# Performance work log

Hardware: AMD Instinct MI355X
Metric: run time of the kernel (lower is better)

Reference implementation:

```python
import jax, jax.numpy as jnp
import numpy as np

S = 8192      # total packed tokens
H = 1152      # hidden size
NH = 16       # heads
HD = 72       # head dim
NSEG = 8      # number of packed (equal-length) sequences
L = S // NSEG # tokens per sequence
SCALE = HD ** -0.5


def setup_inputs() -> dict:
    key = jax.random.key(0)
    ks = jax.random.split(key, 4)
    hidden_states = jax.random.normal(ks[0], (1, S, H), jnp.float32)
    # Real rotary cos/sin per token position within each sequence.
    inv_freq = 1.0 / (10000.0 ** (np.arange(0, HD, 2, dtype=np.float64) / HD))
    freqs = np.outer(np.arange(L, dtype=np.float64), inv_freq)  # [L, HD/2]
    emb = np.concatenate([freqs, freqs], axis=-1)               # [L, HD]
    cos = jnp.asarray(np.tile(np.cos(emb), (NSEG, 1)), jnp.float32)  # [S, HD]
    sin = jnp.asarray(np.tile(np.sin(emb), (NSEG, 1)), jnp.float32)
    Wqkv = jax.random.normal(ks[1], (H, 3 * H), jnp.float32) * (H ** -0.5)
    bqkv = jnp.zeros((3 * H,), jnp.float32)
    Wout = jax.random.normal(ks[2], (H, H), jnp.float32) * (H ** -0.5)
    bout = jnp.zeros((H,), jnp.float32)
    cu_seqlens = jnp.arange(NSEG + 1, dtype=jnp.int32) * L
    return dict(hidden_states=hidden_states, cos=cos, sin=sin,
                Wqkv=Wqkv, bqkv=bqkv, Wout=Wout, bout=bout,
                cu_seqlens=cu_seqlens)


def _rotate_half(x):
    return jnp.concatenate([-x[..., HD // 2:], x[..., :HD // 2]], axis=-1)


def reference(hidden_states, cos, sin, Wqkv, bqkv, Wout, bout, cu_seqlens):
    # QKV projection (fused)
    qkv = hidden_states @ Wqkv + bqkv                 # [1, S, 3H]
    q, k, v = jnp.split(qkv, [H, 2 * H], axis=-1)
    q = q.reshape(1, S, NH, HD)
    k = k.reshape(1, S, NH, HD)
    v = v.reshape(1, S, NH, HD)
    # Inline RoPE on q/k (cos/sin broadcast over heads)
    c = cos[None, :, None, :]
    s = sin[None, :, None, :]
    q = q * c + _rotate_half(q) * s
    k = k * c + _rotate_half(k) * s
    # Varlen (block-diagonal) non-causal attention: equal-length segments
    q = q.reshape(NSEG, L, NH, HD)
    k = k.reshape(NSEG, L, NH, HD)
    v = v.reshape(NSEG, L, NH, HD)
    scores = jnp.einsum('nqhd,nkhd->nhqk', q, k) * SCALE  # [NSEG, NH, L, L]
    probs = jax.nn.softmax(scores, axis=-1)
    ctx = jnp.einsum('nhqk,nkhd->nqhd', probs, v)         # [NSEG, L, NH, HD]
    ctx = ctx.reshape(1, S, H)
    # Output projection
    return ctx @ Wout + bout
```

## Files before the change

### kernel.cpp

```cpp
#include <hip/hip_runtime.h>
#include <hip/hip_fp16.h>
#include <cstdint>

typedef _Float16 half8 __attribute__((ext_vector_type(8)));
typedef _Float16 half4 __attribute__((ext_vector_type(4)));
typedef float floatx4 __attribute__((ext_vector_type(4)));

#define S_TOT 8192
#define H_DIM 1152
#define NHEAD 16
#define HD 72
#define QSTR 96
#define KSTR 104
#define PSTR 76
#define VSTR 76
#define VT_TILE 6080
#define NSEG 8
#define SEGL 1024
#define QSCALE 0.17002324631230988f

__device__ __forceinline__ void gld_lds16(const void* g, void* l) {
  __builtin_amdgcn_global_load_lds((const __attribute__((address_space(1))) void*)g,
                                   (__attribute__((address_space(3))) void*)l, 16, 0, 0);
}

__global__ void cast_f32_f16(const float* __restrict__ in, _Float16* __restrict__ out, int n) {
  int i = (blockIdx.x * 256 + threadIdx.x) * 4;
  if (i < n) {
    float4 v = *(const float4*)(in + i);
    half4 o = { (_Float16)v.x, (_Float16)v.y, (_Float16)v.z, (_Float16)v.w };
    *(half4*)(out + i) = o;
  }
}

__global__ void transpose_cast(const float* __restrict__ W, _Float16* __restrict__ Wt,
                               int R, int C) {
  __shared__ float tile[32][33];
  int tx = threadIdx.x, ty = threadIdx.y;
  int bx = blockIdx.x, by = blockIdx.y;
#pragma unroll
  for (int i = 0; i < 4; ++i)
    tile[ty + i * 8][tx] = W[(size_t)(by * 32 + ty + i * 8) * C + bx * 32 + tx];
  __syncthreads();
#pragma unroll
  for (int i = 0; i < 4; ++i)
    Wt[(size_t)(bx * 32 + ty + i * 8) * R + by * 32 + tx] = (_Float16)tile[tx][ty + i * 8];
}

template <bool OUT_HALF>
__global__ __launch_bounds__(512, 2) void gemm256(
    const _Float16* __restrict__ A, const _Float16* __restrict__ Bt,
    const float* __restrict__ bias, float* __restrict__ Cf, _Float16* __restrict__ Ch,
    int M, int N, int K, int NT) {
  extern __shared__ half8 smem8[];
  char* smem = (char*)smem8;
  const int tid = threadIdx.x;
  const int lane = tid & 63;
  const int w = tid >> 6;
  const int quad = lane >> 4, l16 = lane & 15;
  const int wm = w >> 2, wn = w & 3;

  const int orig = blockIdx.x;
  const int xcd = orig & 7, widx = orig >> 3;
  const int mt = xcd * 4 + (widx & 3), nt = widx >> 2;
  const int m0 = mt * 256, n0 = nt * 256;

  const _Float16* pA[2];
  const _Float16* pB[2];
#pragma unroll
  for (int i = 0; i < 2; ++i) {
    int c = i * 512 + tid;
    int r = c >> 2, cs = c & 3;
    int col = ((cs ^ ((r >> 1) & 3)) << 3);
    pA[i] = A + (size_t)(m0 + r) * K + col;
    int br = n0 + r; if (br >= N) br = N - 1;
    pB[i] = Bt + (size_t)br * K + col;
  }
  const int st0 = tid * 16, st1 = tid * 16 + 8192;
  const int rsl = ((quad ^ ((l16 >> 1) & 3)) << 4);
  const int aoff = (wm * 128 + l16) * 64 + rsl;
  const int boff = 16384 + (wn * 64 + l16) * 64 + rsl;

  half8 afA[8], bfA[4], afB[8], bfB[4];
  floatx4 acc[8][4] = {};

#define STG_A(ds, kcol) { \
  gld_lds16(pA[0] + (kcol), smem + (ds) * 32768 + st0); \
  gld_lds16(pA[1] + (kcol), smem + (ds) * 32768 + st1); }
#define STG_B(ds, kcol) { \
  gld_lds16(pB[0] + (kcol), smem + (ds) * 32768 + 16384 + st0); \
  gld_lds16(pB[1] + (kcol), smem + (ds) * 32768 + 16384 + st1); }
#define LDB4(s, bfx) { \
  _Pragma("unroll") for (int in = 0; in < 4; ++in) \
    bfx[in] = *(const half8*)(smem + (s) * 32768 + boff + in * 1024); }
#define LDA8(s, afx) { \
  _Pragma("unroll") for (int j = 0; j < 8; ++j) \
    afx[j] = *(const half8*)(smem + (s) * 32768 + aoff + j * 1024); }
#define MFMA32(afx, bfx) { \
  __builtin_amdgcn_s_setprio(1); \
  _Pragma("unroll") for (int j = 0; j < 8; ++j) \
  _Pragma("unroll") for (int in = 0; in < 4; ++in) \
    acc[j][in] = \
      __builtin_amdgcn_mfma_f32_16x16x32_f16(afx[j], bfx[in], acc[j][in], 0, 0, 0); \
  __builtin_amdgcn_s_setprio(0); }
#define BAR() __builtin_amdgcn_s_barrier()
#define SBAR() __builtin_amdgcn_sched_barrier(0)
#define LGKM0() { asm volatile("s_waitcnt lgkmcnt(0)" ::: "memory"); SBAR(); }
#define VMWAIT(t) { \
  if ((t) + 3 < KT)        { asm volatile("s_waitcnt vmcnt(4)" ::: "memory"); } \
  else if ((t) + 3 == KT)  { asm volatile("s_waitcnt vmcnt(0)" ::: "memory"); } }

  STG_A(0, 0);  STG_B(0, 0);
  STG_A(1, 32); STG_B(1, 32);
  STG_A(2, 64); STG_B(2, 64);
  asm volatile("s_waitcnt vmcnt(4)" ::: "memory");
  BAR();
  LDB4(0, bfA); LDA8(0, afA);
  LGKM0();

  const int KT = K >> 5;
#pragma unroll 1
  for (int u = 0; u < KT; u += 2) {
    {
      const int rs = (u + 1) & 3, ws = (u + 3) & 3;
      LDB4(rs, bfB); LDA8(rs, afB);
      if (u + 3 < KT) { STG_A(ws, (u + 3) * 32); STG_B(ws, (u + 3) * 32); }
      SBAR();
      MFMA32(afA, bfA);
      SBAR();
      LGKM0();
      VMWAIT(u);
      BAR();
    }
    {
      const int rs = (u + 2) & 3, ws = (u + 4) & 3;
      if (u + 2 < KT) { LDB4(rs, bfA); LDA8(rs, afA); }
      if (u + 4 < KT) { STG_A(ws, (u + 4) * 32); STG_B(ws, (u + 4) * 32); }
      SBAR();
      MFMA32(afB, bfB);
      SBAR();
      LGKM0();
      VMWAIT(u + 1);
      if (u + 2 < KT) BAR();
    }
  }
#undef STG_A
#undef STG_B
#undef LDB4
#undef LDA8
#undef MFMA32
#undef BAR
#undef SBAR
#undef LGKM0
#undef VMWAIT

#pragma unroll
  for (int im = 0; im < 8; ++im) {
    int m = m0 + wm * 128 + im * 16 + quad * 4;
#pragma unroll
    for (int in = 0; in < 4; ++in) {
      int n = n0 + wn * 64 + in * 16 + l16;
      if (n < N) {
        float b = bias[n];
#pragma unroll
        for (int r = 0; r < 4; ++r) {
          float v = acc[im][in][r] + b;
          if (OUT_HALF) Ch[(size_t)(m + r) * N + n] = (_Float16)v;
          else          Cf[(size_t)(m + r) * N + n] = v;
        }
      }
    }
  }
}

__global__ void rope_scatter(const _Float16* __restrict__ QKV,
                             const float* __restrict__ cosb,
                             const float* __restrict__ sinb,
                             _Float16* __restrict__ Qo, _Float16* __restrict__ Ko) {
  int t = blockIdx.x * 256 + threadIdx.x;
  int l = t & 1023, h = (t >> 10) & 15, n = t >> 14;
  int s = n * SEGL + l;
  const _Float16* q = QKV + (size_t)s * 3456 + h * HD;
  const _Float16* k = q + H_DIM;
  const float* cs = cosb + (size_t)s * HD;
  const float* sn = sinb + (size_t)s * HD;
  size_t qo = (size_t)t * QSTR, ko = (size_t)t * KSTR;
  half8 z = {};
  {
    _Float16 qr[72], qv[72];
#pragma unroll
    for (int i = 0; i < 9; ++i) *(half8*)&qr[8 * i] = *(const half8*)(q + 8 * i);
#pragma unroll
    for (int d = 0; d < 36; ++d) {
      float c0 = cs[d], s0 = sn[d], c1 = cs[d + 36], s1 = sn[d + 36];
      float a = (float)qr[d], b = (float)qr[d + 36];
      qv[d]      = (_Float16)((a * c0 - b * s0) * QSCALE);
      qv[d + 36] = (_Float16)((b * c1 + a * s1) * QSCALE);
    }
#pragma unroll
    for (int i = 0; i < 9; ++i) *(half8*)(Qo + qo + 8 * i) = *(half8*)&qv[8 * i];
#pragma unroll
    for (int i = 9; i < 12; ++i) *(half8*)(Qo + qo + 8 * i) = z;
  }
  {
    _Float16 kr[72], kv[72];
#pragma unroll
    for (int i = 0; i < 9; ++i) *(half8*)&kr[8 * i] = *(const half8*)(k + 8 * i);
#pragma unroll
    for (int d = 0; d < 36; ++d) {
      float c0 = cs[d], s0 = sn[d], c1 = cs[d + 36], s1 = sn[d + 36];
      float a = (float)kr[d], b = (float)kr[d + 36];
      kv[d]      = (_Float16)(a * c0 - b * s0);
      kv[d + 36] = (_Float16)(b * c1 + a * s1);
    }
#pragma unroll
    for (int i = 0; i < 9; ++i) *(half8*)(Ko + ko + 8 * i) = *(half8*)&kv[8 * i];
#pragma unroll
    for (int i = 9; i < 13; ++i) *(half8*)(Ko + ko + 8 * i) = z;
  }
}

__global__ __launch_bounds__(256) void transpose_v(const _Float16* __restrict__ QKV,
                                                   _Float16* __restrict__ Vt) {
  __shared__ __align__(16) _Float16 Vs[64 * 88];
  const int tid = threadIdx.x;
  const int kb = blockIdx.x, h = blockIdx.y, n = blockIdx.z;
  const int s0 = n * SEGL + kb * 64;
  const _Float16* src = QKV + (size_t)s0 * 3456 + 2 * H_DIM + h * HD;
  for (int idx = tid; idx < 576; idx += 256) {
    int key = idx / 9, c = idx - key * 9;
    *(half8*)&Vs[key * 88 + c * 8] = *(const half8*)(src + (size_t)key * 3456 + c * 8);
  }
  __syncthreads();
  _Float16* dst = Vt + (((size_t)(n * NHEAD + h)) * 16 + kb) * VT_TILE;
  for (int idx = tid; idx < 800; idx += 256) {
    int d = idx / 10, c = idx - d * 10;
    if (c < 8) {
      half8 v = {};
      if (d < HD) {
#pragma unroll
        for (int j = 0; j < 8; ++j) v[j] = Vs[(c * 8 + j) * 88 + d];
      } else if (d == HD) {
#pragma unroll
        for (int j = 0; j < 8; ++j) v[j] = (_Float16)1.0f;
      }
      *(half8*)(dst + d * VSTR + c * 8) = v;
    } else if (c == 8) {
      *(half8*)(dst + d * VSTR + 64) = half8{};
    } else {
      *(half4*)(dst + d * VSTR + 72) = half4{};
    }
  }
}

__global__ __launch_bounds__(256, 3) void attn_kernel(
    const _Float16* __restrict__ Qb, const _Float16* __restrict__ Kb,
    const _Float16* __restrict__ Vtb, _Float16* __restrict__ Ctx) {
  __shared__ __align__(16) _Float16 Kt[64 * KSTR];
  __shared__ __align__(16) _Float16 Vt[80 * VSTR];
  __shared__ __align__(16) _Float16 Ps[4 * 16 * PSTR];
  const int tid = threadIdx.x;
  const int lane = tid & 63, w = tid >> 6;
  const int quad = lane >> 4, l16 = lane & 15;
  const int id = blockIdx.x;
  const int hn = id & 127, qb = id >> 7;
  const int h = hn >> 3, n = hn & 7;
  const size_t hseg = (size_t)(n * NHEAD + h);
  const _Float16* Qg = Qb + hseg * SEGL * QSTR;
  const _Float16* Kg = Kb + hseg * SEGL * KSTR;
  const _Float16* Vg = Vtb + hseg * 16 * VT_TILE;

  half8 qf[2][3];
#pragma unroll
  for (int qg = 0; qg < 2; ++qg) {
    int row = qb * 128 + w * 32 + qg * 16 + l16;
#pragma unroll
    for (int kc = 0; kc < 3; ++kc)
      qf[qg][kc] = *(const half8*)(Qg + (size_t)row * QSTR + kc * 32 + quad * 8);
  }
  floatx4 o_acc[2][5] = {};

  for (int kb = 0; kb < SEGL / 64; ++kb) {
    __syncthreads();
    {
      const char* base = (const char*)(Kg + (size_t)kb * 64 * KSTR);
#pragma unroll
      for (int i = 0; i < 3; ++i)
        gld_lds16(base + tid * 16 + i * 4096, (char*)Kt + tid * 16 + i * 4096);
      if (tid < 64)
        gld_lds16(base + 12288 + tid * 16, (char*)Kt + 12288 + tid * 16);
    }
    {
      const char* base = (const char*)(Vg + (size_t)kb * VT_TILE);
#pragma unroll
      for (int i = 0; i < 2; ++i)
        gld_lds16(base + tid * 16 + i * 4096, (char*)Vt + tid * 16 + i * 4096);
      if (tid < 248)
        gld_lds16(base + 8192 + tid * 16, (char*)Vt + 8192 + tid * 16);
    }
    __syncthreads();
    floatx4 sa[2][4] = {};
#pragma unroll
    for (int nt = 0; nt < 4; ++nt) {
      half8 kf[3];
#pragma unroll
      for (int kc = 0; kc < 3; ++kc)
        kf[kc] = *(const half8*)&Kt[(nt * 16 + l16) * KSTR + kc * 32 + quad * 8];
#pragma unroll
      for (int qg = 0; qg < 2; ++qg)
#pragma unroll
        for (int kc = 0; kc < 3; ++kc)
          sa[qg][nt] = __builtin_amdgcn_mfma_f32_16x16x32_f16(kf[kc], qf[qg][kc], sa[qg][nt], 0, 0, 0);
    }
#pragma unroll
    for (int qg = 0; qg < 2; ++qg)
#pragma unroll
      for (int nt = 0; nt < 4; ++nt)
#pragma unroll
        for (int r = 0; r < 4; ++r)
          sa[qg][nt][r] = exp2f(sa[qg][nt][r]);
    half8 vf[2][5];
#pragma unroll
    for (int kc2 = 0; kc2 < 2; ++kc2)
#pragma unroll
      for (int t = 0; t < 5; ++t)
        vf[kc2][t] = *(const half8*)&Vt[(t * 16 + l16) * VSTR + kc2 * 32 + quad * 8];
#pragma unroll
    for (int qg = 0; qg < 2; ++qg) {
      int prow = (w * 16 + l16) * PSTR;
#pragma unroll
      for (int nt = 0; nt < 4; ++nt) {
        half4 ph = { (_Float16)sa[qg][nt][0], (_Float16)sa[qg][nt][1],
                     (_Float16)sa[qg][nt][2], (_Float16)sa[qg][nt][3] };
        *(half4*)&Ps[prow + nt * 16 + quad * 4] = ph;
      }
#pragma unroll
      for (int kc2 = 0; kc2 < 2; ++kc2) {
        half8 pb = *(const half8*)&Ps[(w * 16 + l16) * PSTR + kc2 * 32 + quad * 8];
#pragma unroll
        for (int t = 0; t < 5; ++t)
          o_acc[qg][t] = __builtin_amdgcn_mfma_f32_16x16x32_f16(vf[kc2][t], pb, o_acc[qg][t], 0, 0, 0);
      }
    }
  }
#pragma unroll
  for (int qg = 0; qg < 2; ++qg) {
    float lsum = __shfl(o_acc[qg][4][0], 32 + l16, 64);
    float rl = 1.0f / lsum;
    size_t s2 = (size_t)n * SEGL + qb * 128 + w * 32 + qg * 16 + l16;
#pragma unroll
    for (int t = 0; t < 5; ++t) {
      int d0 = t * 16 + quad * 4;
      if (d0 < HD) {
        half4 hv = { (_Float16)(o_acc[qg][t][0] * rl), (_Float16)(o_acc[qg][t][1] * rl),
                     (_Float16)(o_acc[qg][t][2] * rl), (_Float16)(o_acc[qg][t][3] * rl) };
        *(half4*)&Ctx[s2 * H_DIM + h * HD + d0] = hv;
      }
    }
  }
}

extern "C" void kernel_launch(void* const* d_in, const int* in_sizes, int n_in,
                              void* d_out, int out_size, void* d_ws, size_t ws_size,
                              hipStream_t stream) {
  const float* X    = (const float*)d_in[0];
  const float* cosb = (const float*)d_in[1];
  const float* sinb = (const float*)d_in[2];
  const float* Wqkv = (const float*)d_in[3];
  const float* bqkv = (const float*)d_in[4];
  const float* Wout = (const float*)d_in[5];
  const float* bout = (const float*)d_in[6];
  float* out = (float*)d_out;
  char* ws = (char*)d_ws;

  _Float16* Xb   = (_Float16*)(ws);
  _Float16* Wqt  = (_Float16*)(ws + 18874368);
  _Float16* Wot  = (_Float16*)(ws + 26836992);
  _Float16* QKVb = (_Float16*)(ws + 29491200);
  _Float16* Qb   = (_Float16*)(ws + 86114304);
  _Float16* Kb   = (_Float16*)(ws + 111280128);
  _Float16* Vtb  = (_Float16*)(ws + 138543104);
  _Float16* Ctx  = Xb;

  static bool attr_done = false;
  if (!attr_done) {
    hipFuncSetAttribute(reinterpret_cast<const void*>(gemm256<true>),
                        hipFuncAttributeMaxDynamicSharedMemorySize, 131072);
    hipFuncSetAttribute(reinterpret_cast<const void*>(gemm256<false>),
                        hipFuncAttributeMaxDynamicSharedMemorySize, 131072);
    attr_done = true;
  }

  cast_f32_f16<<<9216, 256, 0, stream>>>(X, Xb, S_TOT * H_DIM);
  transpose_cast<<<dim3(108, 36), dim3(32, 8), 0, stream>>>(Wqkv, Wqt, H_DIM, 3 * H_DIM);
  transpose_cast<<<dim3(36, 36), dim3(32, 8), 0, stream>>>(Wout, Wot, H_DIM, H_DIM);
  gemm256<true><<<448, 512, 131072, stream>>>(Xb, Wqt, bqkv, nullptr, QKVb,
                                              S_TOT, 3 * H_DIM, H_DIM, 14);
  rope_scatter<<<512, 256, 0, stream>>>(QKVb, cosb, sinb, Qb, Kb);
  transpose_v<<<dim3(16, 16, 8), 256, 0, stream>>>(QKVb, Vtb);
  attn_kernel<<<1024, 256, 0, stream>>>(Qb, Kb, Vtb, Ctx);
  gemm256<false><<<160, 512, 131072, stream>>>(Ctx, Wot, bout, out, nullptr,
                                               S_TOT, H_DIM, H_DIM, 5);
}
```

Baseline: 385.8 us.

## Stage RoPE outputs through LDS for coalesced stores; raise wave priority around MFMA

The RoPE scatter kernel now writes each thread's rotated Q/K row into shared memory, then has the block store the contiguous output region in coalesced 16-byte chunks. Before, each thread wrote its own strided row. Separately, the attention kernel wraps its two MFMA loops in s_setprio(1)/s_setprio(0) so waves issuing matrix ops get scheduling priority. In exchange, the RoPE kernel uses 60KB of LDS per block plus extra barriers, which may lower its occupancy.

Result: faster. 359.6 us (-6.8%).

```diff
diff --git a/kernel.cpp b/kernel.cpp
--- a/kernel.cpp
+++ b/kernel.cpp
@@ -173,18 +173,21 @@
   }
 }
 
-__global__ void rope_scatter(const _Float16* __restrict__ QKV,
-                             const float* __restrict__ cosb,
-                             const float* __restrict__ sinb,
-                             _Float16* __restrict__ Qo, _Float16* __restrict__ Ko) {
-  int t = blockIdx.x * 256 + threadIdx.x;
-  int l = t & 1023, h = (t >> 10) & 15, n = t >> 14;
-  int s = n * SEGL + l;
+__global__ __launch_bounds__(256) void rope_scatter(
+    const _Float16* __restrict__ QKV,
+    const float* __restrict__ cosb,
+    const float* __restrict__ sinb,
+    _Float16* __restrict__ Qo, _Float16* __restrict__ Ko) {
+  __shared__ __align__(16) _Float16 Ls[256 * 120];
+  const int tid = threadIdx.x;
+  const int t0 = blockIdx.x * 256;
+  const int t = t0 + tid;
+  const int l = t & 1023, h = (t >> 10) & 15, n = t >> 14;
+  const int s = n * SEGL + l;
   const _Float16* q = QKV + (size_t)s * 3456 + h * HD;
   const _Float16* k = q + H_DIM;
   const float* cs = cosb + (size_t)s * HD;
   const float* sn = sinb + (size_t)s * HD;
-  size_t qo = (size_t)t * QSTR, ko = (size_t)t * KSTR;
   half8 z = {};
   {
     _Float16 qr[72], qv[72];
@@ -198,10 +201,21 @@
       qv[d + 36] = (_Float16)((b * c1 + a * s1) * QSCALE);
     }
 #pragma unroll
-    for (int i = 0; i < 9; ++i) *(half8*)(Qo + qo + 8 * i) = *(half8*)&qv[8 * i];
-#pragma unroll
-    for (int i = 9; i < 12; ++i) *(half8*)(Qo + qo + 8 * i) = z;
-  }
+    for (int i = 0; i < 9; ++i) *(half8*)&Ls[tid * 104 + 8 * i] = *(half8*)&qv[8 * i];
+#pragma unroll
+    for (int i = 9; i < 12; ++i) *(half8*)&Ls[tid * 104 + 8 * i] = z;
+  }
+  __syncthreads();
+  {
+    _Float16* dst = Qo + (size_t)t0 * QSTR;
+#pragma unroll
+    for (int it = 0; it < 12; ++it) {
+      int j = tid + it * 256;
+      int row = j / 12, c = j - row * 12;
+      *(half8*)(dst + (size_t)j * 8) = *(const half8*)&Ls[row * 104 + c * 8];
+    }
+  }
+  __syncthreads();
   {
     _Float16 kr[72], kv[72];
 #pragma unroll
@@ -214,9 +228,19 @@
       kv[d + 36] = (_Float16)(b * c1 + a * s1);
     }
 #pragma unroll
-    for (int i = 0; i < 9; ++i) *(half8*)(Ko + ko + 8 * i) = *(half8*)&kv[8 * i];
-#pragma unroll
-    for (int i = 9; i < 13; ++i) *(half8*)(Ko + ko + 8 * i) = z;
+    for (int i = 0; i < 9; ++i) *(half8*)&Ls[tid * 120 + 8 * i] = *(half8*)&kv[8 * i];
+#pragma unroll
+    for (int i = 9; i < 13; ++i) *(half8*)&Ls[tid * 120 + 8 * i] = z;
+  }
+  __syncthreads();
+  {
+    _Float16* dst = Ko + (size_t)t0 * KSTR;
+#pragma unroll
+    for (int it = 0; it < 13; ++it) {
+      int j = tid + it * 256;
+      int row = j / 13, c = j - row * 13;
+      *(half8*)(dst + (size_t)j * 8) = *(const half8*)&Ls[row * 120 + c * 8];
+    }
   }
 }
 
@@ -300,6 +324,7 @@
     }
     __syncthreads();
     floatx4 sa[2][4] = {};
+    __builtin_amdgcn_s_setprio(1);
 #pragma unroll
     for (int nt = 0; nt < 4; ++nt) {
       half8 kf[3];
@@ -312,6 +337,7 @@
         for (int kc = 0; kc < 3; ++kc)
           sa[qg][nt] = __builtin_amdgcn_mfma_f32_16x16x32_f16(kf[kc], qf[qg][kc], sa[qg][nt], 0, 0, 0);
     }
+    __builtin_amdgcn_s_setprio(0);
 #pragma unroll
     for (int qg = 0; qg < 2; ++qg)
 #pragma unroll
@@ -334,6 +360,7 @@
                      (_Float16)sa[qg][nt][2], (_Float16)sa[qg][nt][3] };
         *(half4*)&Ps[prow + nt * 16 + quad * 4] = ph;
       }
+      __builtin_amdgcn_s_setprio(1);
 #pragma unroll
       for (int kc2 = 0; kc2 < 2; ++kc2) {
         half8 pb = *(const half8*)&Ps[(w * 16 + l16) * PSTR + kc2 * 32 + quad * 8];
@@ -341,6 +368,7 @@
         for (int t = 0; t < 5; ++t)
           o_acc[qg][t] = __builtin_amdgcn_mfma_f32_16x16x32_f16(vf[kc2][t], pb, o_acc[qg][t], 0, 0, 0);
       }
+      __builtin_amdgcn_s_setprio(0);
     }
   }
 #pragma unroll
```
